# Kernel tuning notes

Measured on AMD Instinct MI355X. Metric: run time of the kernel, lower is better.

Reference implementation:

```python
import jax, jax.numpy as jnp
import numpy as np

EPS = 1e-5


def ternarize(w):
    # TWN: delta = 0.7*mean|w|; alpha = mean of |w| over entries above delta
    delta = 0.7 * jnp.mean(jnp.abs(w))
    mask = (jnp.abs(w) > delta).astype(w.dtype)
    alpha = jnp.sum(jnp.abs(w) * mask) / jnp.maximum(jnp.sum(mask), 1.0)
    q = alpha * jnp.sign(w) * mask
    # straight-through estimator (matches torch `w + (q - w).detach()`)
    return w + jax.lax.stop_gradient(q - w)


def conv2d(x, w, stride, pad):
    # x: NCHW, w: OIHW
    return jax.lax.conv_general_dilated(
        x, w, window_strides=(stride, stride), padding=[(pad, pad), (pad, pad)],
        dimension_numbers=("NCHW", "OIHW", "NCHW"))


def batchnorm(x, gamma, beta, mean, var):
    # inference-mode BN over channel dim of NCHW
    inv = gamma / jnp.sqrt(var + EPS)
    return x * inv[None, :, None, None] + (beta - mean * inv)[None, :, None, None]


def setup_inputs() -> dict:
    key = jax.random.key(0)
    ks = jax.random.split(key, 12)
    d = {
        "x": jax.random.normal(ks[0], (64, 3, 224, 224), jnp.float32),
        "w1": jax.random.normal(ks[1], (32, 3, 3, 3), jnp.float32) * 0.1,
        "g1": jnp.ones((32,), jnp.float32), "b1": jnp.zeros((32,), jnp.float32),
        "m1": jax.random.normal(ks[2], (32,), jnp.float32) * 0.1,
        "v1": jax.random.uniform(ks[3], (32,), jnp.float32, 0.5, 1.5),
        "w2": jax.random.normal(ks[4], (64, 32, 3, 3), jnp.float32) * 0.05,
        "g2": jnp.ones((64,), jnp.float32), "b2": jnp.zeros((64,), jnp.float32),
        "m2": jax.random.normal(ks[5], (64,), jnp.float32) * 0.1,
        "v2": jax.random.uniform(ks[6], (64,), jnp.float32, 0.5, 1.5),
        "w3": jax.random.normal(ks[7], (128, 64, 3, 3), jnp.float32) * 0.05,
        "g3": jnp.ones((128,), jnp.float32), "b3": jnp.zeros((128,), jnp.float32),
        "m3": jax.random.normal(ks[8], (128,), jnp.float32) * 0.1,
        "v3": jax.random.uniform(ks[9], (128,), jnp.float32, 0.5, 1.5),
        "wl": jax.random.normal(ks[10], (10, 128), jnp.float32) * 0.1,
        "bl": jax.random.normal(ks[11], (10,), jnp.float32) * 0.01,
    }
    return d


def reference(x, w1, g1, b1, m1, v1, w2, g2, b2, m2, v2,
              w3, g3, b3, m3, v3, wl, bl):
    h = jax.nn.relu(batchnorm(conv2d(x, ternarize(w1), 2, 1), g1, b1, m1, v1))
    h = jax.nn.relu(batchnorm(conv2d(h, ternarize(w2), 1, 1), g2, b2, m2, v2))
    h = jax.nn.relu(batchnorm(conv2d(h, ternarize(w3), 2, 1), g3, b3, m3, v3))
    h = jnp.mean(h, axis=(2, 3))  # AdaptiveAvgPool2d((1,1)) + flatten -> [N,128]
    return h @ ternarize(wl).T + bl
```

## Files before the change

kernel.cpp:

```cpp
#include <hip/hip_runtime.h>
#include <cstddef>

typedef __attribute__((ext_vector_type(8))) short short8;
typedef __attribute__((ext_vector_type(4))) float floatx4;

__device__ __forceinline__ unsigned short f2bf(float f) {
  union { float f; unsigned u; } v; v.f = f;
  const unsigned r = v.u + 0x7fffu + ((v.u >> 16) & 1u);
  return (unsigned short)(r >> 16);
}

__device__ __forceinline__ float block_reduce_sum(float v, float* sm) {
#pragma unroll
  for (int off = 32; off > 0; off >>= 1) v += __shfl_down(v, off, 64);
  const int lane = threadIdx.x & 63, wid = threadIdx.x >> 6;
  __syncthreads();
  if (lane == 0) sm[wid] = v;
  __syncthreads();
  if (threadIdx.x == 0) {
    float t = 0.f;
    const int nw = (blockDim.x + 63) >> 6;
    for (int i = 0; i < nw; ++i) t += sm[i];
    sm[0] = t;
  }
  __syncthreads();
  return sm[0];
}

__device__ __forceinline__ void tsel(int t, const float* w0, const float* w1,
                                     const float* w2, const float* w3, int n0,
                                     int n1, int n2, int n3,
                                     const float*& w, int& n) {
  w = (t == 0) ? w0 : (t == 1) ? w1 : (t == 2) ? w2 : w3;
  n = (t == 0) ? n0 : (t == 1) ? n1 : (t == 2) ? n2 : n3;
}

__global__ __launch_bounds__(256) void tern_phase1(
    const float* w0, const float* w1, const float* w2, const float* w3,
    int n0, int n1, int n2, int n3, float* __restrict__ red) {
  __shared__ float sm[8];
  const float* w; int n;
  tsel(blockIdx.y, w0, w1, w2, w3, n0, n1, n2, n3, w, n);
  if ((int)blockIdx.x * 256 >= n) return;
  const int i = blockIdx.x * 256 + threadIdx.x;
  float s = (i < n) ? fabsf(w[i]) : 0.f;
  s = block_reduce_sum(s, sm);
  if (threadIdx.x == 0) atomicAdd(&red[blockIdx.y * 4 + 0], s);
}

__global__ __launch_bounds__(256) void tern_phase2(
    const float* w0, const float* w1, const float* w2, const float* w3,
    int n0, int n1, int n2, int n3, float* __restrict__ red,
    unsigned short* __restrict__ bp1, unsigned short* __restrict__ bp2,
    unsigned short* __restrict__ bp3, float* __restrict__ ql) {
  __shared__ float sm[8];
  const float* w; int n;
  const int by = blockIdx.y;
  tsel(by, w0, w1, w2, w3, n0, n1, n2, n3, w, n);
  if ((int)blockIdx.x * 256 >= n) return;
  const float delta = 0.7f * red[by * 4 + 0] / (float)n;
  const int i = blockIdx.x * 256 + threadIdx.x;
  float c = 0.f, a = 0.f;
  float wv = 0.f;
  if (i < n) {
    wv = w[i];
    const float av = fabsf(wv);
    if (av > delta) { c = 1.f; a = av; }
  }
  if (i < n) {
    const float sgnf = (wv > delta) ? 1.f : (wv < -delta ? -1.f : 0.f);
    const unsigned short sgnb =
        (wv > delta) ? 0x3F80u : (wv < -delta ? 0xBF80u : 0u);
    if (by == 0) {
      const int k = i % 27, oc = i / 27;
      bp1[((size_t)(k >> 3) * 32 + oc) * 8 + (k & 7)] = sgnb;
    } else if (by == 1) {
      const int k = (i % 9) * 32 + (i % 288) / 9;
      bp2[((size_t)(k >> 3) * 64 + i / 288) * 8 + (k & 7)] = sgnb;
    } else if (by == 2) {
      const int k = (i % 9) * 64 + (i % 576) / 9;
      bp3[((size_t)(k >> 3) * 128 + i / 576) * 8 + (k & 7)] = sgnb;
    } else {
      ql[i] = sgnf;
    }
  }
  c = block_reduce_sum(c, sm);
  a = block_reduce_sum(a, sm);
  if (threadIdx.x == 0) {
    atomicAdd(&red[by * 4 + 1], c);
    atomicAdd(&red[by * 4 + 2], a);
  }
}

__global__ __launch_bounds__(256) void conv1_mfma(
    const float* __restrict__ x, const unsigned short* __restrict__ bp1,
    const float* __restrict__ g1, const float* __restrict__ b1,
    const float* __restrict__ m1, const float* __restrict__ v1,
    const float* __restrict__ red, unsigned short* __restrict__ y) {
  __shared__ float xs[3 * 17 * 33];
  __shared__ unsigned short im[128 * 40];
  const int n = blockIdx.y;
  const int oh0 = (blockIdx.x / 7) * 8, ow0 = (blockIdx.x % 7) * 16;
  const int t = threadIdx.x;
  const int wave = t >> 6, lane = t & 63, quad = lane >> 4, l16 = lane & 15;

  const int ihb = oh0 * 2 - 1, iwb = ow0 * 2 - 1;
  for (int i = t; i < 1683; i += 256) {
    const int ic = i / 561, r2 = i % 561;
    const int pr = r2 / 33, pc = r2 % 33;
    const int ih = ihb + pr, iw = iwb + pc;
    float v = 0.f;
    if ((unsigned)ih < 224u && (unsigned)iw < 224u)
      v = x[((size_t)n * 3 + ic) * 50176 + (size_t)ih * 224 + iw];
    xs[i] = v;
  }
  __syncthreads();

#pragma unroll
  for (int cc = 0; cc < 2; ++cc) {
    const int c = cc * 256 + t;
    const int px = c >> 2, seg = c & 3;
    const int ohl = px >> 4, owl = px & 15;
    unsigned u[4];
#pragma unroll
    for (int jj = 0; jj < 4; ++jj) {
      unsigned short lo = 0, hi = 0;
      const int k0 = seg * 8 + 2 * jj, k1 = k0 + 1;
      if (k0 < 27) {
        const int ic = k0 / 9, tp = k0 % 9;
        lo = f2bf(xs[(ic * 17 + ohl * 2 + tp / 3) * 33 + owl * 2 + tp % 3]);
      }
      if (k1 < 27) {
        const int ic = k1 / 9, tp = k1 % 9;
        hi = f2bf(xs[(ic * 17 + ohl * 2 + tp / 3) * 33 + owl * 2 + tp % 3]);
      }
      u[jj] = (unsigned)lo | ((unsigned)hi << 16);
    }
    *(uint4*)(&im[px * 40 + seg * 8]) = make_uint4(u[0], u[1], u[2], u[3]);
  }

  short8 bfr[2];
#pragma unroll
  for (int nf = 0; nf < 2; ++nf)
    bfr[nf] = *(const short8*)(bp1 + ((size_t)quad * 32 + nf * 16 + l16) * 8);

  floatx4 acc[2][2];
#pragma unroll
  for (int mi = 0; mi < 2; ++mi) {
    acc[mi][0] = (floatx4){0.f, 0.f, 0.f, 0.f};
    acc[mi][1] = (floatx4){0.f, 0.f, 0.f, 0.f};
  }
  __syncthreads();

#pragma unroll
  for (int mi = 0; mi < 2; ++mi) {
    const int pxb = (wave * 2 + mi) * 16;
    const short8 a = *(const short8*)(&im[(pxb + l16) * 40 + quad * 8]);
#pragma unroll
    for (int nf = 0; nf < 2; ++nf)
      acc[mi][nf] = __builtin_amdgcn_mfma_f32_16x16x32_bf16(
          a, bfr[nf], acc[mi][nf], 0, 0, 0);
  }

  const float alpha1 = red[2] / fmaxf(red[1], 1.f);
  float sc[2], bs[2];
#pragma unroll
  for (int nf = 0; nf < 2; ++nf) {
    const int ch = nf * 16 + l16;
    const float inv = g1[ch] / sqrtf(v1[ch] + 1e-5f);
    sc[nf] = alpha1 * inv;
    bs[nf] = b1[ch] - m1[ch] * inv;
  }
  __syncthreads();
#pragma unroll
  for (int mi = 0; mi < 2; ++mi) {
    const int ohl = wave * 2 + mi;
#pragma unroll
    for (int r = 0; r < 4; ++r) {
      const int px = ohl * 16 + quad * 4 + r;
#pragma unroll
      for (int nf = 0; nf < 2; ++nf) {
        const float vv = fmaxf(acc[mi][nf][r] * sc[nf] + bs[nf], 0.f);
        im[px * 40 + ((nf * 16 + l16) ^ (quad * 8))] = f2bf(vv);
      }
    }
  }
  __syncthreads();
#pragma unroll
  for (int i = 0; i < 2; ++i) {
    const int c = i * 256 + t;
    const int px = c >> 2, cg = c & 3;
    const int ohl = px >> 4, owl = px & 15;
    const uint4 v =
        *(const uint4*)(&im[px * 40 + ((cg ^ ((px >> 2) & 3)) * 8)]);
    *(uint4*)(y + (((size_t)n * 112 + oh0 + ohl) * 112 + ow0 + owl) * 32 +
              cg * 8) = v;
  }
}

__global__ __launch_bounds__(256, 2) void conv23_fused(
    const unsigned short* __restrict__ act1,
    const unsigned short* __restrict__ bp2,
    const unsigned short* __restrict__ bp3,
    const float* __restrict__ g2, const float* __restrict__ b2,
    const float* __restrict__ m2, const float* __restrict__ v2,
    const float* __restrict__ g3, const float* __restrict__ b3,
    const float* __restrict__ m3, const float* __restrict__ v3,
    const float* __restrict__ red, float* __restrict__ pooled) {
  constexpr int HS = 2504;
  __shared__ unsigned short shbuf[8 * HS];
  __shared__ float pbuf[128];
  unsigned short* a1p = shbuf;
  unsigned short* c2o = shbuf;
  const int t = threadIdx.x;
  const int img = blockIdx.y;
  const int ty = blockIdx.x / 7, tx = blockIdx.x % 7;
  const int wave = t >> 6, lane = t & 63, quad = lane >> 4, l16 = lane & 15;
  const int h0 = ty * 16 - 1, w0 = tx * 16 - 1;

  for (int c = t; c < 19 * 19 * 4; c += 256) {
    const int seg = c & 3, pix = c >> 2;
    const int ri = pix / 19, rj = pix % 19;
    const int ih = h0 - 1 + ri, iw = w0 - 1 + rj;
    uint4 v = make_uint4(0u, 0u, 0u, 0u);
    if ((unsigned)ih < 112u && (unsigned)iw < 112u)
      v = *(const uint4*)(act1 + (((size_t)img * 112 + ih) * 112 + iw) * 32 +
                          seg * 8);
    *(uint4*)(&a1p[((seg * 19 + ri) * 19 + rj) * 8]) = v;
  }

  int abase[5];
#pragma unroll
  for (int s = 0; s < 5; ++s) {
    const int mt = wave + s * 4;
    int apx = mt * 16 + l16;
    if (apx > 288) apx = 288;
    const int pi = apx / 17, pj = apx % 17;
    abase[s] = ((quad * 19 + pi) * 19 + pj) * 8;
  }
  floatx4 acc2[5][4];
#pragma unroll
  for (int s = 0; s < 5; ++s)
#pragma unroll
    for (int nf = 0; nf < 4; ++nf) acc2[s][nf] = (floatx4){0.f, 0.f, 0.f, 0.f};

  short8 bcur[4], bnxt[4];
#pragma unroll
  for (int nf = 0; nf < 4; ++nf)
    bcur[nf] = *(const short8*)(bp2 + ((size_t)quad * 64 + nf * 16 + l16) * 8);
  __syncthreads();

#pragma unroll
  for (int tap = 0; tap < 9; ++tap) {
    const int kh = tap / 3, kw = tap % 3;
    if (tap + 1 < 9) {
      const int kg = (tap + 1) * 4 + quad;
#pragma unroll
      for (int nf = 0; nf < 4; ++nf)
        bnxt[nf] =
            *(const short8*)(bp2 + ((size_t)kg * 64 + nf * 16 + l16) * 8);
    }
    const int toff = (kh * 19 + kw) * 8;
#pragma unroll
    for (int s = 0; s < 5; ++s) {
      const short8 a = *(const short8*)(&a1p[abase[s] + toff]);
#pragma unroll
      for (int nf = 0; nf < 4; ++nf)
        acc2[s][nf] = __builtin_amdgcn_mfma_f32_16x16x32_bf16(
            a, bcur[nf], acc2[s][nf], 0, 0, 0);
    }
#pragma unroll
    for (int nf = 0; nf < 4; ++nf) bcur[nf] = bnxt[nf];
  }
  __syncthreads();

  const float alpha2 = red[6] / fmaxf(red[5], 1.f);
  float sc[4], bs[4];
#pragma unroll
  for (int nf = 0; nf < 4; ++nf) {
    const int ch = nf * 16 + l16;
    const float inv = g2[ch] / sqrtf(v2[ch] + 1e-5f);
    sc[nf] = alpha2 * inv;
    bs[nf] = b2[ch] - m2[ch] * inv;
  }
  const int lo8 = l16 & 7, hs0 = l16 >> 3;
#pragma unroll
  for (int s = 0; s < 5; ++s) {
    const int mt = wave + s * 4;
#pragma unroll
    for (int r = 0; r < 4; ++r) {
      const int px = mt * 16 + quad * 4 + r;
      if (px <= 288) {
        const int pi = px / 17, pj = px % 17;
        const int slot = (pj >> 1) + (pj & 1) * 9;
        const bool inb =
            ((unsigned)(h0 + pi) < 112u) && ((unsigned)(w0 + pj) < 112u);
#pragma unroll
        for (int nf = 0; nf < 4; ++nf) {
          const float vv =
              inb ? fmaxf(acc2[s][nf][r] * sc[nf] + bs[nf], 0.f) : 0.f;
          c2o[(nf * 2 + hs0) * HS + (pi * 18 + slot) * 8 + lo8] = f2bf(vv);
        }
      }
    }
  }
  __syncthreads();

  int a3off[4];
#pragma unroll
  for (int mf = 0; mf < 4; ++mf) {
    const int px = mf * 16 + l16;
    a3off[mf] = quad * HS + (((px >> 3) * 2) * 18 + (px & 7)) * 8;
  }
  floatx4 acc3[4][2];
#pragma unroll
  for (int mf = 0; mf < 4; ++mf) {
    acc3[mf][0] = (floatx4){0.f, 0.f, 0.f, 0.f};
    acc3[mf][1] = (floatx4){0.f, 0.f, 0.f, 0.f};
  }
  short8 b3c0, b3c1, b3n0, b3n1;
  {
    const int kg = quad;
    b3c0 = *(const short8*)(bp3 + ((size_t)kg * 128 + wave * 32 + l16) * 8);
    b3c1 =
        *(const short8*)(bp3 + ((size_t)kg * 128 + wave * 32 + 16 + l16) * 8);
  }
#pragma unroll
  for (int u = 0; u < 18; ++u) {
    const int H = u / 9, tap = u % 9;
    const int kh = tap / 3, kw = tap % 3;
    if (u + 1 < 18) {
      const int H2 = (u + 1) / 9, tap2 = (u + 1) % 9;
      const int kg = tap2 * 8 + H2 * 4 + quad;
      b3n0 = *(const short8*)(bp3 + ((size_t)kg * 128 + wave * 32 + l16) * 8);
      b3n1 = *(const short8*)(bp3 +
                              ((size_t)kg * 128 + wave * 32 + 16 + l16) * 8);
    }
    const int toff = (kh * 18 + (kw >> 1) + (kw & 1) * 9) * 8 + H * 4 * HS;
#pragma unroll
    for (int mf = 0; mf < 4; ++mf) {
      const short8 a = *(const short8*)(&c2o[a3off[mf] + toff]);
      acc3[mf][0] = __builtin_amdgcn_mfma_f32_16x16x32_bf16(
          a, b3c0, acc3[mf][0], 0, 0, 0);
      acc3[mf][1] = __builtin_amdgcn_mfma_f32_16x16x32_bf16(
          a, b3c1, acc3[mf][1], 0, 0, 0);
    }
    b3c0 = b3n0; b3c1 = b3n1;
  }

  const float alpha3 = red[10] / fmaxf(red[9], 1.f);
#pragma unroll
  for (int nf = 0; nf < 2; ++nf) {
    const int ch = wave * 32 + nf * 16 + l16;
    const float inv = g3[ch] / sqrtf(v3[ch] + 1e-5f);
    const float scv = alpha3 * inv, bsv = b3[ch] - m3[ch] * inv;
    float s = 0.f;
#pragma unroll
    for (int mf = 0; mf < 4; ++mf)
#pragma unroll
      for (int rr = 0; rr < 4; ++rr)
        s += fmaxf(acc3[mf][nf][rr] * scv + bsv, 0.f);
    s += __shfl_xor(s, 16);
    s += __shfl_xor(s, 32);
    if (lane < 16) pbuf[ch] = s;
  }
  __syncthreads();
  if (t < 128) atomicAdd(&pooled[(size_t)img * 128 + t], pbuf[t]);
}

__global__ void linear_kernel(const float* __restrict__ pooled,
                              const float* __restrict__ ql,
                              const float* __restrict__ bl,
                              const float* __restrict__ red,
                              float* __restrict__ out) {
  const int idx = blockIdx.x * blockDim.x + threadIdx.x;
  if (idx >= 64 * 10) return;
  const int n = idx / 10, o = idx % 10;
  const float* p = pooled + (size_t)n * 128;
  const float* w = ql + (size_t)o * 128;
  float s = 0.f;
#pragma unroll 4
  for (int c = 0; c < 128; ++c) s += p[c] * w[c];
  const float alpha_l = red[14] / fmaxf(red[13], 1.f);
  out[idx] = s * (alpha_l / 3136.f) + bl[o];
}

extern "C" void kernel_launch(void* const* d_in, const int* in_sizes, int n_in,
                              void* d_out, int out_size, void* d_ws,
                              size_t ws_size, hipStream_t stream) {
  const float* x  = (const float*)d_in[0];
  const float* w1 = (const float*)d_in[1];
  const float* g1 = (const float*)d_in[2];
  const float* b1 = (const float*)d_in[3];
  const float* m1 = (const float*)d_in[4];
  const float* v1 = (const float*)d_in[5];
  const float* w2 = (const float*)d_in[6];
  const float* g2 = (const float*)d_in[7];
  const float* b2 = (const float*)d_in[8];
  const float* m2 = (const float*)d_in[9];
  const float* v2 = (const float*)d_in[10];
  const float* w3 = (const float*)d_in[11];
  const float* g3 = (const float*)d_in[12];
  const float* b3 = (const float*)d_in[13];
  const float* m3 = (const float*)d_in[14];
  const float* v3 = (const float*)d_in[15];
  const float* wl = (const float*)d_in[16];
  const float* bl = (const float*)d_in[17];
  float* out = (float*)d_out;

  float* Wf = (float*)d_ws;
  float* red = Wf;
  float* pooled = red + 16;
  float* bp1f = pooled + 8192;
  float* ql = bp1f + 512;
  unsigned short* bp1 = (unsigned short*)bp1f;
  unsigned short* Us = (unsigned short*)(ql + 1280);
  unsigned short* bp2 = Us;
  unsigned short* bp3 = bp2 + 18432;
  unsigned short* act1 = bp3 + 73728;

  hipMemsetAsync(red, 0, (16 + 8192 + 512) * sizeof(float), stream);
  tern_phase1<<<dim3(288, 4), 256, 0, stream>>>(w1, w2, w3, wl, 864, 18432,
                                                73728, 1280, red);
  tern_phase2<<<dim3(288, 4), 256, 0, stream>>>(w1, w2, w3, wl, 864, 18432,
                                                73728, 1280, red, bp1, bp2,
                                                bp3, ql);

  conv1_mfma<<<dim3(98, 64), 256, 0, stream>>>(x, bp1, g1, b1, m1, v1, red,
                                               act1);
  conv23_fused<<<dim3(49, 64), 256, 0, stream>>>(act1, bp2, bp3, g2, b2, m2,
                                                 v2, g3, b3, m3, v3, red,
                                                 pooled);
  linear_kernel<<<3, 256, 0, stream>>>(pooled, ql, bl, red, out);
}
```

Before: 238.7 us.

## Fuse conv1 into the conv2/conv3 kernel, recomputing the halo in shared memory

Removes the separate conv1 kernel and its bf16 activation buffer in global memory. Each conv23 block now loads a 39x39x3 input patch, builds the conv1 im2col in LDS and runs conv1 MFMAs for the 19x19 halo tile, writing post-BN/ReLU values directly into the conv2 input layout. This avoids writing and re-reading the roughly 51 MB act1 tensor, at the cost of recomputing halo pixels and using more shared memory per block, which may reduce occupancy.

New measurement: 292.7 us. 22.6% more time.

```diff
diff --git a/kernel.cpp b/kernel.cpp
--- a/kernel.cpp
+++ b/kernel.cpp
@@ -92,141 +92,101 @@
   }
 }
 
-__global__ __launch_bounds__(256) void conv1_mfma(
+__global__ __launch_bounds__(256, 2) void conv123_fused(
     const float* __restrict__ x, const unsigned short* __restrict__ bp1,
+    const unsigned short* __restrict__ bp2,
+    const unsigned short* __restrict__ bp3,
     const float* __restrict__ g1, const float* __restrict__ b1,
     const float* __restrict__ m1, const float* __restrict__ v1,
-    const float* __restrict__ red, unsigned short* __restrict__ y) {
-  __shared__ float xs[3 * 17 * 33];
-  __shared__ unsigned short im[128 * 40];
-  const int n = blockIdx.y;
-  const int oh0 = (blockIdx.x / 7) * 8, ow0 = (blockIdx.x % 7) * 16;
-  const int t = threadIdx.x;
-  const int wave = t >> 6, lane = t & 63, quad = lane >> 4, l16 = lane & 15;
-
-  const int ihb = oh0 * 2 - 1, iwb = ow0 * 2 - 1;
-  for (int i = t; i < 1683; i += 256) {
-    const int ic = i / 561, r2 = i % 561;
-    const int pr = r2 / 33, pc = r2 % 33;
-    const int ih = ihb + pr, iw = iwb + pc;
-    float v = 0.f;
-    if ((unsigned)ih < 224u && (unsigned)iw < 224u)
-      v = x[((size_t)n * 3 + ic) * 50176 + (size_t)ih * 224 + iw];
-    xs[i] = v;
-  }
-  __syncthreads();
-
-#pragma unroll
-  for (int cc = 0; cc < 2; ++cc) {
-    const int c = cc * 256 + t;
-    const int px = c >> 2, seg = c & 3;
-    const int ohl = px >> 4, owl = px & 15;
-    unsigned u[4];
-#pragma unroll
-    for (int jj = 0; jj < 4; ++jj) {
-      unsigned short lo = 0, hi = 0;
-      const int k0 = seg * 8 + 2 * jj, k1 = k0 + 1;
-      if (k0 < 27) {
-        const int ic = k0 / 9, tp = k0 % 9;
-        lo = f2bf(xs[(ic * 17 + ohl * 2 + tp / 3) * 33 + owl * 2 + tp % 3]);
-      }
-      if (k1 < 27) {
-        const int ic = k1 / 9, tp = k1 % 9;
-        hi = f2bf(xs[(ic * 17 + ohl * 2 + tp / 3) * 33 + owl * 2 + tp % 3]);
-      }
-      u[jj] = (unsigned)lo | ((unsigned)hi << 16);
-    }
-    *(uint4*)(&im[px * 40 + seg * 8]) = make_uint4(u[0], u[1], u[2], u[3]);
-  }
-
-  short8 bfr[2];
-#pragma unroll
-  for (int nf = 0; nf < 2; ++nf)
-    bfr[nf] = *(const short8*)(bp1 + ((size_t)quad * 32 + nf * 16 + l16) * 8);
-
-  floatx4 acc[2][2];
-#pragma unroll
-  for (int mi = 0; mi < 2; ++mi) {
-    acc[mi][0] = (floatx4){0.f, 0.f, 0.f, 0.f};
-    acc[mi][1] = (floatx4){0.f, 0.f, 0.f, 0.f};
-  }
-  __syncthreads();
-
-#pragma unroll
-  for (int mi = 0; mi < 2; ++mi) {
-    const int pxb = (wave * 2 + mi) * 16;
-    const short8 a = *(const short8*)(&im[(pxb + l16) * 40 + quad * 8]);
-#pragma unroll
-    for (int nf = 0; nf < 2; ++nf)
-      acc[mi][nf] = __builtin_amdgcn_mfma_f32_16x16x32_bf16(
-          a, bfr[nf], acc[mi][nf], 0, 0, 0);
-  }
-
-  const float alpha1 = red[2] / fmaxf(red[1], 1.f);
-  float sc[2], bs[2];
-#pragma unroll
-  for (int nf = 0; nf < 2; ++nf) {
-    const int ch = nf * 16 + l16;
-    const float inv = g1[ch] / sqrtf(v1[ch] + 1e-5f);
-    sc[nf] = alpha1 * inv;
-    bs[nf] = b1[ch] - m1[ch] * inv;
-  }
-  __syncthreads();
-#pragma unroll
-  for (int mi = 0; mi < 2; ++mi) {
-    const int ohl = wave * 2 + mi;
-#pragma unroll
-    for (int r = 0; r < 4; ++r) {
-      const int px = ohl * 16 + quad * 4 + r;
-#pragma unroll
-      for (int nf = 0; nf < 2; ++nf) {
-        const float vv = fmaxf(acc[mi][nf][r] * sc[nf] + bs[nf], 0.f);
-        im[px * 40 + ((nf * 16 + l16) ^ (quad * 8))] = f2bf(vv);
-      }
-    }
-  }
-  __syncthreads();
-#pragma unroll
-  for (int i = 0; i < 2; ++i) {
-    const int c = i * 256 + t;
-    const int px = c >> 2, cg = c & 3;
-    const int ohl = px >> 4, owl = px & 15;
-    const uint4 v =
-        *(const uint4*)(&im[px * 40 + ((cg ^ ((px >> 2) & 3)) * 8)]);
-    *(uint4*)(y + (((size_t)n * 112 + oh0 + ohl) * 112 + ow0 + owl) * 32 +
-              cg * 8) = v;
-  }
-}
-
-__global__ __launch_bounds__(256, 2) void conv23_fused(
-    const unsigned short* __restrict__ act1,
-    const unsigned short* __restrict__ bp2,
-    const unsigned short* __restrict__ bp3,
     const float* __restrict__ g2, const float* __restrict__ b2,
     const float* __restrict__ m2, const float* __restrict__ v2,
     const float* __restrict__ g3, const float* __restrict__ b3,
     const float* __restrict__ m3, const float* __restrict__ v3,
     const float* __restrict__ red, float* __restrict__ pooled) {
   constexpr int HS = 2504;
-  __shared__ unsigned short shbuf[8 * HS];
+  __shared__ unsigned short shbuf[26272];
   __shared__ float pbuf[128];
   unsigned short* a1p = shbuf;
+  unsigned short* im = shbuf + 11552;
+  float* xs = (float*)shbuf;
   unsigned short* c2o = shbuf;
   const int t = threadIdx.x;
   const int img = blockIdx.y;
   const int ty = blockIdx.x / 7, tx = blockIdx.x % 7;
   const int wave = t >> 6, lane = t & 63, quad = lane >> 4, l16 = lane & 15;
   const int h0 = ty * 16 - 1, w0 = tx * 16 - 1;
-
-  for (int c = t; c < 19 * 19 * 4; c += 256) {
-    const int seg = c & 3, pix = c >> 2;
-    const int ri = pix / 19, rj = pix % 19;
-    const int ih = h0 - 1 + ri, iw = w0 - 1 + rj;
-    uint4 v = make_uint4(0u, 0u, 0u, 0u);
-    if ((unsigned)ih < 112u && (unsigned)iw < 112u)
-      v = *(const uint4*)(act1 + (((size_t)img * 112 + ih) * 112 + iw) * 32 +
-                          seg * 8);
-    *(uint4*)(&a1p[((seg * 19 + ri) * 19 + rj) * 8]) = v;
+  const int xr0 = 32 * ty - 5, xc0 = 32 * tx - 5;
+
+  for (int i = t; i < 4563; i += 256) {
+    const int ic = i / 1521, r2 = i % 1521;
+    const int pr = r2 / 39, pc = r2 % 39;
+    const int xr = xr0 + pr, xc = xc0 + pc;
+    float v = 0.f;
+    if ((unsigned)xr < 224u && (unsigned)xc < 224u)
+      v = x[((size_t)img * 3 + ic) * 50176 + (size_t)xr * 224 + xc];
+    xs[i] = v;
+  }
+  __syncthreads();
+
+  for (int c = t; c < 1472; c += 256) {
+    const int px = c >> 2, seg = c & 3;
+    const int ri = px / 19, rj = px % 19;
+    unsigned u[4];
+#pragma unroll
+    for (int jj = 0; jj < 4; ++jj) {
+      unsigned short lo = 0, hi = 0;
+      const int k0 = seg * 8 + 2 * jj, k1 = k0 + 1;
+      if (px < 361 && k0 < 27) {
+        const int ic = k0 / 9, tp = k0 % 9;
+        lo = f2bf(xs[(ic * 39 + 2 * ri + tp / 3) * 39 + 2 * rj + tp % 3]);
+      }
+      if (px < 361 && k1 < 27) {
+        const int ic = k1 / 9, tp = k1 % 9;
+        hi = f2bf(xs[(ic * 39 + 2 * ri + tp / 3) * 39 + 2 * rj + tp % 3]);
+      }
+      u[jj] = (unsigned)lo | ((unsigned)hi << 16);
+    }
+    *(uint4*)(&im[px * 40 + seg * 8]) = make_uint4(u[0], u[1], u[2], u[3]);
+  }
+  short8 b1f[2];
+#pragma unroll
+  for (int nf = 0; nf < 2; ++nf)
+    b1f[nf] = *(const short8*)(bp1 + ((size_t)quad * 32 + nf * 16 + l16) * 8);
+  const float alpha1 = red[2] / fmaxf(red[1], 1.f);
+  float sc1[2], bs1[2];
+#pragma unroll
+  for (int nf = 0; nf < 2; ++nf) {
+    const int ch = nf * 16 + l16;
+    const float inv = g1[ch] / sqrtf(v1[ch] + 1e-5f);
+    sc1[nf] = alpha1 * inv;
+    bs1[nf] = b1[ch] - m1[ch] * inv;
+  }
+  __syncthreads();
+
+#pragma unroll
+  for (int s = 0; s < 6; ++s) {
+    const int mt = wave + s * 4;
+    int apx = mt * 16 + l16;
+    if (apx > 367) apx = 367;
+    const short8 a = *(const short8*)(&im[apx * 40 + quad * 8]);
+    floatx4 ac0 = (floatx4){0.f, 0.f, 0.f, 0.f};
+    floatx4 ac1 = (floatx4){0.f, 0.f, 0.f, 0.f};
+    ac0 = __builtin_amdgcn_mfma_f32_16x16x32_bf16(a, b1f[0], ac0, 0, 0, 0);
+    ac1 = __builtin_amdgcn_mfma_f32_16x16x32_bf16(a, b1f[1], ac1, 0, 0, 0);
+    const int sg0 = l16 >> 3, e0 = l16 & 7;
+#pragma unroll
+    for (int r = 0; r < 4; ++r) {
+      const int px = mt * 16 + quad * 4 + r;
+      if (px < 361) {
+        const int ri = px / 19, rj = px % 19;
+        const bool inb = ((unsigned)(h0 - 1 + ri) < 112u) &&
+                         ((unsigned)(w0 - 1 + rj) < 112u);
+        const float v0 = inb ? fmaxf(ac0[r] * sc1[0] + bs1[0], 0.f) : 0.f;
+        const float v1v = inb ? fmaxf(ac1[r] * sc1[1] + bs1[1], 0.f) : 0.f;
+        a1p[(((0 * 2 + sg0) * 19 + ri) * 19 + rj) * 8 + e0] = f2bf(v0);
+        a1p[(((1 * 2 + sg0) * 19 + ri) * 19 + rj) * 8 + e0] = f2bf(v1v);
+      }
+    }
   }
 
   int abase[5];
@@ -417,7 +377,6 @@
   unsigned short* Us = (unsigned short*)(ql + 1280);
   unsigned short* bp2 = Us;
   unsigned short* bp3 = bp2 + 18432;
-  unsigned short* act1 = bp3 + 73728;
 
   hipMemsetAsync(red, 0, (16 + 8192 + 512) * sizeof(float), stream);
   tern_phase1<<<dim3(288, 4), 256, 0, stream>>>(w1, w2, w3, wl, 864, 18432,
@@ -426,10 +385,8 @@
                                                 73728, 1280, red, bp1, bp2,
                                                 bp3, ql);
 
-  conv1_mfma<<<dim3(98, 64), 256, 0, stream>>>(x, bp1, g1, b1, m1, v1, red,
-                                               act1);
-  conv23_fused<<<dim3(49, 64), 256, 0, stream>>>(act1, bp2, bp3, g2, b2, m2,
-                                                 v2, g3, b3, m3, v3, red,
-                                                 pooled);
+  conv123_fused<<<dim3(49, 64), 256, 0, stream>>>(
+      x, bp1, bp2, bp3, g1, b1, m1, v1, g2, b2, m2, v2, g3, b3, m3, v3, red,
+      pooled);
   linear_kernel<<<3, 256, 0, stream>>>(pooled, ql, bl, red, out);
 }
```

## Split fused conv2/conv3 into two channel halves to cut registers and LDS

Applied to the files above, without the earlier changes.

Conv2's 64 output channels are now computed in two passes of 32. After each pass the half is written to a smaller shared buffer and immediately consumed by the matching half of conv3's reduction. This shrinks live accumulator registers and shared memory (separate a1p and half-size c2h buffers instead of one 8*HS union), and launch bounds are raised from 2 to 3 blocks per CU to get more occupancy. The cost is an extra barrier and two sequential phases per block, which may reduce the overlap within each wave.

Result: slower. 246.7 us (+3.4%).

```diff
diff --git a/kernel.cpp b/kernel.cpp
--- a/kernel.cpp
+++ b/kernel.cpp
@@ -198,7 +198,7 @@
   }
 }
 
-__global__ __launch_bounds__(256, 2) void conv23_fused(
+__global__ __launch_bounds__(256, 3) void conv23_fused(
     const unsigned short* __restrict__ act1,
     const unsigned short* __restrict__ bp2,
     const unsigned short* __restrict__ bp3,
@@ -208,10 +208,9 @@
     const float* __restrict__ m3, const float* __restrict__ v3,
     const float* __restrict__ red, float* __restrict__ pooled) {
   constexpr int HS = 2504;
-  __shared__ unsigned short shbuf[8 * HS];
+  __shared__ unsigned short a1p[11552];
+  __shared__ unsigned short c2h[4 * HS];
   __shared__ float pbuf[128];
-  unsigned short* a1p = shbuf;
-  unsigned short* c2o = shbuf;
   const int t = threadIdx.x;
   const int img = blockIdx.y;
   const int ty = blockIdx.x / 7, tx = blockIdx.x % 7;
@@ -238,74 +237,6 @@
     const int pi = apx / 17, pj = apx % 17;
     abase[s] = ((quad * 19 + pi) * 19 + pj) * 8;
   }
-  floatx4 acc2[5][4];
-#pragma unroll
-  for (int s = 0; s < 5; ++s)
-#pragma unroll
-    for (int nf = 0; nf < 4; ++nf) acc2[s][nf] = (floatx4){0.f, 0.f, 0.f, 0.f};
-
-  short8 bcur[4], bnxt[4];
-#pragma unroll
-  for (int nf = 0; nf < 4; ++nf)
-    bcur[nf] = *(const short8*)(bp2 + ((size_t)quad * 64 + nf * 16 + l16) * 8);
-  __syncthreads();
-
-#pragma unroll
-  for (int tap = 0; tap < 9; ++tap) {
-    const int kh = tap / 3, kw = tap % 3;
-    if (tap + 1 < 9) {
-      const int kg = (tap + 1) * 4 + quad;
-#pragma unroll
-      for (int nf = 0; nf < 4; ++nf)
-        bnxt[nf] =
-            *(const short8*)(bp2 + ((size_t)kg * 64 + nf * 16 + l16) * 8);
-    }
-    const int toff = (kh * 19 + kw) * 8;
-#pragma unroll
-    for (int s = 0; s < 5; ++s) {
-      const short8 a = *(const short8*)(&a1p[abase[s] + toff]);
-#pragma unroll
-      for (int nf = 0; nf < 4; ++nf)
-        acc2[s][nf] = __builtin_amdgcn_mfma_f32_16x16x32_bf16(
-            a, bcur[nf], acc2[s][nf], 0, 0, 0);
-    }
-#pragma unroll
-    for (int nf = 0; nf < 4; ++nf) bcur[nf] = bnxt[nf];
-  }
-  __syncthreads();
-
-  const float alpha2 = red[6] / fmaxf(red[5], 1.f);
-  float sc[4], bs[4];
-#pragma unroll
-  for (int nf = 0; nf < 4; ++nf) {
-    const int ch = nf * 16 + l16;
-    const float inv = g2[ch] / sqrtf(v2[ch] + 1e-5f);
-    sc[nf] = alpha2 * inv;
-    bs[nf] = b2[ch] - m2[ch] * inv;
-  }
-  const int lo8 = l16 & 7, hs0 = l16 >> 3;
-#pragma unroll
-  for (int s = 0; s < 5; ++s) {
-    const int mt = wave + s * 4;
-#pragma unroll
-    for (int r = 0; r < 4; ++r) {
-      const int px = mt * 16 + quad * 4 + r;
-      if (px <= 288) {
-        const int pi = px / 17, pj = px % 17;
-        const int slot = (pj >> 1) + (pj & 1) * 9;
-        const bool inb =
-            ((unsigned)(h0 + pi) < 112u) && ((unsigned)(w0 + pj) < 112u);
-#pragma unroll
-        for (int nf = 0; nf < 4; ++nf) {
-          const float vv =
-              inb ? fmaxf(acc2[s][nf][r] * sc[nf] + bs[nf], 0.f) : 0.f;
-          c2o[(nf * 2 + hs0) * HS + (pi * 18 + slot) * 8 + lo8] = f2bf(vv);
-        }
-      }
-    }
-  }
-  __syncthreads();
-
   int a3off[4];
 #pragma unroll
   for (int mf = 0; mf < 4; ++mf) {
@@ -318,34 +249,104 @@
     acc3[mf][0] = (floatx4){0.f, 0.f, 0.f, 0.f};
     acc3[mf][1] = (floatx4){0.f, 0.f, 0.f, 0.f};
   }
-  short8 b3c0, b3c1, b3n0, b3n1;
-  {
-    const int kg = quad;
-    b3c0 = *(const short8*)(bp3 + ((size_t)kg * 128 + wave * 32 + l16) * 8);
-    b3c1 =
-        *(const short8*)(bp3 + ((size_t)kg * 128 + wave * 32 + 16 + l16) * 8);
-  }
-#pragma unroll
-  for (int u = 0; u < 18; ++u) {
-    const int H = u / 9, tap = u % 9;
-    const int kh = tap / 3, kw = tap % 3;
-    if (u + 1 < 18) {
-      const int H2 = (u + 1) / 9, tap2 = (u + 1) % 9;
-      const int kg = tap2 * 8 + H2 * 4 + quad;
-      b3n0 = *(const short8*)(bp3 + ((size_t)kg * 128 + wave * 32 + l16) * 8);
-      b3n1 = *(const short8*)(bp3 +
+  const int lo8 = l16 & 7, hs0 = l16 >> 3;
+  const float alpha2 = red[6] / fmaxf(red[5], 1.f);
+  __syncthreads();
+
+#pragma unroll
+  for (int p = 0; p < 2; ++p) {
+    floatx4 acc2[5][2];
+#pragma unroll
+    for (int s = 0; s < 5; ++s) {
+      acc2[s][0] = (floatx4){0.f, 0.f, 0.f, 0.f};
+      acc2[s][1] = (floatx4){0.f, 0.f, 0.f, 0.f};
+    }
+    short8 bcur[2], bnxt[2];
+#pragma unroll
+    for (int nf = 0; nf < 2; ++nf)
+      bcur[nf] = *(const short8*)(
+          bp2 + ((size_t)quad * 64 + p * 32 + nf * 16 + l16) * 8);
+#pragma unroll
+    for (int tap = 0; tap < 9; ++tap) {
+      const int kh = tap / 3, kw = tap % 3;
+      if (tap + 1 < 9) {
+        const int kg = (tap + 1) * 4 + quad;
+#pragma unroll
+        for (int nf = 0; nf < 2; ++nf)
+          bnxt[nf] = *(const short8*)(
+              bp2 + ((size_t)kg * 64 + p * 32 + nf * 16 + l16) * 8);
+      }
+      const int toff = (kh * 19 + kw) * 8;
+#pragma unroll
+      for (int s = 0; s < 5; ++s) {
+        const short8 a = *(const short8*)(&a1p[abase[s] + toff]);
+#pragma unroll
+        for (int nf = 0; nf < 2; ++nf)
+          acc2[s][nf] = __builtin_amdgcn_mfma_f32_16x16x32_bf16(
+              a, bcur[nf], acc2[s][nf], 0, 0, 0);
+      }
+#pragma unroll
+      for (int nf = 0; nf < 2; ++nf) bcur[nf] = bnxt[nf];
+    }
+    float sc[2], bs[2];
+#pragma unroll
+    for (int nf = 0; nf < 2; ++nf) {
+      const int ch = p * 32 + nf * 16 + l16;
+      const float inv = g2[ch] / sqrtf(v2[ch] + 1e-5f);
+      sc[nf] = alpha2 * inv;
+      bs[nf] = b2[ch] - m2[ch] * inv;
+    }
+#pragma unroll
+    for (int s = 0; s < 5; ++s) {
+      const int mt = wave + s * 4;
+#pragma unroll
+      for (int r = 0; r < 4; ++r) {
+        const int px = mt * 16 + quad * 4 + r;
+        if (px <= 288) {
+          const int pi = px / 17, pj = px % 17;
+          const int slot = (pj >> 1) + (pj & 1) * 9;
+          const bool inb =
+              ((unsigned)(h0 + pi) < 112u) && ((unsigned)(w0 + pj) < 112u);
+#pragma unroll
+          for (int nf = 0; nf < 2; ++nf) {
+            const float vv =
+                inb ? fmaxf(acc2[s][nf][r] * sc[nf] + bs[nf], 0.f) : 0.f;
+            c2h[(nf * 2 + hs0) * HS + (pi * 18 + slot) * 8 + lo8] = f2bf(vv);
+          }
+        }
+      }
+    }
+    __syncthreads();
+
+    short8 b3c0, b3c1, b3n0, b3n1;
+    {
+      const int kg = p * 4 + quad;
+      b3c0 = *(const short8*)(bp3 + ((size_t)kg * 128 + wave * 32 + l16) * 8);
+      b3c1 = *(const short8*)(bp3 +
                               ((size_t)kg * 128 + wave * 32 + 16 + l16) * 8);
     }
-    const int toff = (kh * 18 + (kw >> 1) + (kw & 1) * 9) * 8 + H * 4 * HS;
-#pragma unroll
-    for (int mf = 0; mf < 4; ++mf) {
-      const short8 a = *(const short8*)(&c2o[a3off[mf] + toff]);
-      acc3[mf][0] = __builtin_amdgcn_mfma_f32_16x16x32_bf16(
-          a, b3c0, acc3[mf][0], 0, 0, 0);
-      acc3[mf][1] = __builtin_amdgcn_mfma_f32_16x16x32_bf16(
-          a, b3c1, acc3[mf][1], 0, 0, 0);
-    }
-    b3c0 = b3n0; b3c1 = b3n1;
+#pragma unroll
+    for (int tap = 0; tap < 9; ++tap) {
+      const int kh = tap / 3, kw = tap % 3;
+      if (tap + 1 < 9) {
+        const int kg = (tap + 1) * 8 + p * 4 + quad;
+        b3n0 =
+            *(const short8*)(bp3 + ((size_t)kg * 128 + wave * 32 + l16) * 8);
+        b3n1 = *(const short8*)(bp3 +
+                                ((size_t)kg * 128 + wave * 32 + 16 + l16) * 8);
+      }
+      const int toff = (kh * 18 + (kw >> 1) + (kw & 1) * 9) * 8;
+#pragma unroll
+      for (int mf = 0; mf < 4; ++mf) {
+        const short8 a = *(const short8*)(&c2h[a3off[mf] + toff]);
+        acc3[mf][0] = __builtin_amdgcn_mfma_f32_16x16x32_bf16(
+            a, b3c0, acc3[mf][0], 0, 0, 0);
+        acc3[mf][1] = __builtin_amdgcn_mfma_f32_16x16x32_bf16(
+            a, b3c1, acc3[mf][1], 0, 0, 0);
+      }
+      b3c0 = b3n0; b3c1 = b3n1;
+    }
+    if (p == 0) __syncthreads();
   }
 
   const float alpha3 = red[10] / fmaxf(red[9], 1.f);
```
